# Kernel tuning notes

Measured on AMD Instinct MI355X. Metric: run time of the kernel, lower is better.

The kernel has to match this reference:

```python
import jax, jax.numpy as jnp
import numpy as np

D_MODEL = 1024
NHEAD = 16
HEAD_DIM = D_MODEL // NHEAD


def setup_inputs() -> dict:
    key = jax.random.key(0)
    ks = jax.random.split(key, 11)
    B, S, D = 4, 2048, D_MODEL
    scale = 1.0 / np.sqrt(D)
    inp = {
        'q': jax.random.normal(ks[0], (B, S, D), jnp.float32),
        'k': jax.random.normal(ks[1], (B, S, D), jnp.float32),
        'v': jax.random.normal(ks[2], (B, S, D), jnp.float32),
        'Wq': jax.random.normal(ks[3], (D, D), jnp.float32) * scale,
        'bq': jnp.zeros((D,), jnp.float32),
        'Wk': jax.random.normal(ks[4], (D, D), jnp.float32) * scale,
        'bk': jnp.zeros((D,), jnp.float32),
        'Wv': jax.random.normal(ks[5], (D, D), jnp.float32) * scale,
        'bv': jnp.zeros((D,), jnp.float32),
        'Wo': jax.random.normal(ks[6], (D, D), jnp.float32) * scale,
        'bo': jnp.zeros((D,), jnp.float32),
    }
    return inp


def reference(q, k, v, Wq, bq, Wk, bk, Wv, bv, Wo, bo):
    B, S, D = q.shape
    H, Hd = NHEAD, HEAD_DIM
    # projections (torch Linear: x @ W.T + b), then split heads -> [B,H,S,Hd]
    qh = (q @ Wq.T + bq).reshape(B, S, H, Hd).transpose(0, 2, 1, 3)
    kh = (k @ Wk.T + bk).reshape(B, S, H, Hd).transpose(0, 2, 1, 3)
    vh = (v @ Wv.T + bv).reshape(B, S, H, Hd).transpose(0, 2, 1, 3)
    # scaled dot-product attention (mask=None, dropout eval-mode identity)
    scores = jnp.einsum('bhqd,bhkd->bhqk', qh, kh) / jnp.sqrt(jnp.float32(Hd))
    attn = jax.nn.softmax(scores, axis=-1)
    out = jnp.einsum('bhqk,bhkd->bhqd', attn, vh)  # [B,H,S,Hd]
    out = out.transpose(0, 2, 1, 3).reshape(B, S, D)
    return out @ Wo.T + bo
```

## Files before the change

### kernel.cpp

```cpp
#include <hip/hip_runtime.h>
#include <cstdint>

using u16 = unsigned short;
using u32 = unsigned int;
typedef __bf16 bf16x8 __attribute__((ext_vector_type(8)));
typedef float f32x4 __attribute__((ext_vector_type(4)));
typedef float f32x16 __attribute__((ext_vector_type(16)));
typedef u16 u16x8 __attribute__((ext_vector_type(8)));
typedef u16 u16x4 __attribute__((ext_vector_type(4)));

#define DEV static __device__ __forceinline__

DEV u16 f2bf(float f) {
  uint32_t u = __builtin_bit_cast(uint32_t, f);
  u += 0x7FFFu + ((u >> 16) & 1u);
  return (u16)(u >> 16);
}
DEV float bf2f(u16 h) {
  uint32_t u = ((uint32_t)h) << 16;
  return __builtin_bit_cast(float, u);
}
DEV u32 cvt_pk_bf16(float lo, float hi) {
  u32 r;
  asm("v_cvt_pk_bf16_f32 %0, %1, %2" : "=v"(r) : "v"(lo), "v"(hi));
  return r;
}

typedef const u32 __attribute__((address_space(1))) gcu32;
typedef u32 __attribute__((address_space(3))) lu32;
DEV void gl_lds16(const u16* g, u16* l) {
  __builtin_amdgcn_global_load_lds((gcu32*)g, (lu32*)l, 16, 0, 0);
}

#define MFMA(a, b, c) __builtin_amdgcn_mfma_f32_16x16x32_bf16((a), (b), (c), 0, 0, 0)
#define MFMA32(a, b, c) __builtin_amdgcn_mfma_f32_32x32x16_bf16((a), (b), (c), 0, 0, 0)

__global__ __launch_bounds__(256) void cvt_all(
    const float* __restrict__ q, const float* __restrict__ k,
    const float* __restrict__ v, const float* __restrict__ Wq,
    const float* __restrict__ Wk, const float* __restrict__ Wv,
    const float* __restrict__ Wo, u16* __restrict__ Xb, u16* __restrict__ Wb,
    u16* __restrict__ WoB) {
  const int bid = blockIdx.x;
  const float* src;
  u16* dst;
  size_t i;
  if (bid < 12288) {
    const int z = bid >> 12;
    src = (z == 0) ? q : (z == 1) ? k : v;
    dst = Xb + (size_t)z * 8388608;
    i = ((size_t)(bid & 4095) * 256 + threadIdx.x) * 8;
  } else {
    const int r = bid - 12288;
    const int z = r >> 9;
    src = (z == 0) ? Wq : (z == 1) ? Wk : (z == 2) ? Wv : Wo;
    dst = (z < 3) ? (Wb + (size_t)z * 1048576) : WoB;
    i = ((size_t)(r & 511) * 256 + threadIdx.x) * 8;
  }
  const float4 a = *(const float4*)(src + i);
  const float4 b = *(const float4*)(src + i + 4);
  u16x8 o;
  o[0] = f2bf(a.x); o[1] = f2bf(a.y); o[2] = f2bf(a.z); o[3] = f2bf(a.w);
  o[4] = f2bf(b.x); o[5] = f2bf(b.y); o[6] = f2bf(b.z); o[7] = f2bf(b.w);
  *(u16x8*)(dst + i) = o;
}

__global__ __launch_bounds__(512) void proj_gemm_bf(
    const u16* __restrict__ Xb, const u16* __restrict__ Wb,
    const float* __restrict__ bq, const float* __restrict__ bk,
    const float* __restrict__ bv, u16* __restrict__ Qh, u16* __restrict__ Kh,
    u16* __restrict__ Vt) {
  __shared__ u16 As[256 * 64];
  __shared__ u16 Bs[128 * 64];
  const int z = blockIdx.z;
  const int m0 = blockIdx.y * 256, n0 = blockIdx.x * 128;

  const u16* x = Xb + (size_t)z * 8388608;
  const u16* W = Wb + (size_t)z * 1048576;
  const float* bias = (z == 0) ? bq : (z == 1) ? bk : bv;
  u16* out = (z == 0) ? Qh : (z == 1) ? Kh : Vt;
  const float oscale = (z == 0) ? 0.18033688011112042f : 1.0f;

  const int tid = threadIdx.x;
  const int w = tid >> 6, lane = tid & 63;
  const int wr = w >> 1, wc = w & 1;
  const int lr = lane & 15, lk = (lane >> 4) * 8;

  const u16* xg = x + (size_t)(m0 + w * 8 + (lane >> 3)) * 1024 + (lane & 7) * 8;
  const u16* wg_ = W + (size_t)(n0 + w * 8 + (lane >> 3)) * 1024 + (lane & 7) * 8;

  f32x4 acc[4][4];
  const f32x4 fzero = {0.f, 0.f, 0.f, 0.f};
#pragma unroll
  for (int m = 0; m < 4; ++m)
#pragma unroll
    for (int n = 0; n < 4; ++n) acc[m][n] = fzero;

  for (int kt = 0; kt < 16; ++kt) {
    const int k0 = kt * 64;
    __syncthreads();
#pragma unroll
    for (int c = 0; c < 4; ++c)
      gl_lds16(xg + (size_t)c * 64 * 1024 + k0, &As[c * 4096 + w * 512]);
#pragma unroll
    for (int c = 0; c < 2; ++c)
      gl_lds16(wg_ + (size_t)c * 64 * 1024 + k0, &Bs[c * 4096 + w * 512]);
    asm volatile("s_waitcnt vmcnt(0)" ::: "memory");
    __syncthreads();
#pragma unroll
    for (int kk = 0; kk < 2; ++kk) {
      bf16x8 a[4], b[4];
#pragma unroll
      for (int m = 0; m < 4; ++m)
        a[m] = *(const bf16x8*)&As[(wr * 64 + m * 16 + lr) * 64 + kk * 32 + lk];
#pragma unroll
      for (int n = 0; n < 4; ++n)
        b[n] = *(const bf16x8*)&Bs[(wc * 64 + n * 16 + lr) * 64 + kk * 32 + lk];
#pragma unroll
      for (int m = 0; m < 4; ++m)
#pragma unroll
        for (int n = 0; n < 4; ++n) acc[m][n] = MFMA(a[m], b[n], acc[m][n]);
    }
  }

#pragma unroll
  for (int n = 0; n < 4; ++n) {
    const int col = n0 + wc * 64 + n * 16 + lr;
    const float bvv = bias[col];
    const int h = col >> 6, d = col & 63;
#pragma unroll
    for (int m = 0; m < 4; ++m) {
#pragma unroll
      for (int j = 0; j < 4; ++j) {
        const int rowg = m0 + wr * 64 + m * 16 + (lane >> 4) * 4 + j;
        const int bb = rowg >> 11, s = rowg & 2047;
        const float val = (acc[m][n][j] + bvv) * oscale;
        size_t idx;
        if (z != 2)
          idx = ((size_t)(bb * 16 + h) * 2048 + s) * 64 + d;
        else
          idx = ((size_t)(bb * 16 + h) * 64 + d) * 2048 + s;
        out[idx] = f2bf(val);
      }
    }
  }
}

__global__ __launch_bounds__(256) void proj_gemm_f32(
    const float* __restrict__ q, const float* __restrict__ k,
    const float* __restrict__ v, const float* __restrict__ Wq,
    const float* __restrict__ Wk, const float* __restrict__ Wv,
    const float* __restrict__ bq, const float* __restrict__ bk,
    const float* __restrict__ bv, u16* __restrict__ Qh, u16* __restrict__ Kh,
    u16* __restrict__ Vt) {
  __shared__ u16 As[128][40];
  __shared__ u16 Bs[128][40];
  const int z = blockIdx.z;
  const float* x = (z == 0) ? q : (z == 1) ? k : v;
  const float* W = (z == 0) ? Wq : (z == 1) ? Wk : Wv;
  const float* bias = (z == 0) ? bq : (z == 1) ? bk : bv;
  u16* out = (z == 0) ? Qh : (z == 1) ? Kh : Vt;
  const float oscale = (z == 0) ? 0.18033688011112042f : 1.0f;

  const int tid = threadIdx.x;
  const int m0 = blockIdx.y * 128, n0 = blockIdx.x * 128;
  const int w = tid >> 6, lane = tid & 63;
  const int wr = w >> 1, wc = w & 1;
  const int lr = lane & 15, lk = (lane >> 4) * 8;
  const int srow = tid >> 3, sc4 = (tid & 7) * 4;

  f32x4 acc[4][4];
  const f32x4 fzero = {0.f, 0.f, 0.f, 0.f};
#pragma unroll
  for (int m = 0; m < 4; ++m)
#pragma unroll
    for (int n = 0; n < 4; ++n) acc[m][n] = fzero;

  for (int kt = 0; kt < 32; ++kt) {
    const int k0 = kt * 32;
    __syncthreads();
#pragma unroll
    for (int c = 0; c < 4; ++c) {
      const float4 av = *(const float4*)(x + (size_t)(m0 + c * 32 + srow) * 1024 + k0 + sc4);
      const float4 bvv = *(const float4*)(W + (size_t)(n0 + c * 32 + srow) * 1024 + k0 + sc4);
      u16x4 ah, bh;
      ah[0] = f2bf(av.x); ah[1] = f2bf(av.y); ah[2] = f2bf(av.z); ah[3] = f2bf(av.w);
      bh[0] = f2bf(bvv.x); bh[1] = f2bf(bvv.y); bh[2] = f2bf(bvv.z); bh[3] = f2bf(bvv.w);
      *(u16x4*)&As[c * 32 + srow][sc4] = ah;
      *(u16x4*)&Bs[c * 32 + srow][sc4] = bh;
    }
    __syncthreads();
    bf16x8 a[4], b[4];
#pragma unroll
    for (int m = 0; m < 4; ++m)
      a[m] = *(const bf16x8*)&As[wr * 64 + m * 16 + lr][lk];
#pragma unroll
    for (int n = 0; n < 4; ++n)
      b[n] = *(const bf16x8*)&Bs[wc * 64 + n * 16 + lr][lk];
#pragma unroll
    for (int m = 0; m < 4; ++m)
#pragma unroll
      for (int n = 0; n < 4; ++n) acc[m][n] = MFMA(a[m], b[n], acc[m][n]);
  }

#pragma unroll
  for (int n = 0; n < 4; ++n) {
    const int col = n0 + wc * 64 + n * 16 + lr;
    const float bvv = bias[col];
    const int h = col >> 6, d = col & 63;
#pragma unroll
    for (int m = 0; m < 4; ++m) {
#pragma unroll
      for (int j = 0; j < 4; ++j) {
        const int rowg = m0 + wr * 64 + m * 16 + (lane >> 4) * 4 + j;
        const int bb = rowg >> 11, s = rowg & 2047;
        const float val = (acc[m][n][j] + bvv) * oscale;
        size_t idx;
        if (z != 2)
          idx = ((size_t)(bb * 16 + h) * 2048 + s) * 64 + d;
        else
          idx = ((size_t)(bb * 16 + h) * 64 + d) * 2048 + s;
        out[idx] = f2bf(val);
      }
    }
  }
}

__global__ __launch_bounds__(512, 4) void attn_fwd(
    const u16* __restrict__ Qh, const u16* __restrict__ Kh,
    const u16* __restrict__ Vt, u16* __restrict__ Att) {
  __shared__ u16 Ks[64][72];
  __shared__ u16 Vs[64][72];
  const int tid = threadIdx.x;
  const int w = tid >> 6, lane = tid & 63;
  const int lq = lane & 31, h = lane >> 5;
  const int head = blockIdx.x, q0 = blockIdx.y * 256;
  const u16* Qb = Qh + (size_t)head * 131072;
  const u16* Kb = Kh + (size_t)head * 131072;
  const u16* Vb = Vt + (size_t)head * 131072;
  const int qrow = q0 + w * 32 + lq;

  bf16x8 qf[4];
#pragma unroll
  for (int dc = 0; dc < 4; ++dc)
    qf[dc] = *(const bf16x8*)(Qb + (size_t)qrow * 64 + dc * 16 + h * 8);

  u16x8 ou;
#pragma unroll
  for (int j = 0; j < 8; ++j) ou[j] = 0x3F80;
  const bf16x8 ones = __builtin_bit_cast(bf16x8, ou);

  f32x16 o0 = {}, o1 = {}, osum = {};

  const int srow = tid >> 3, scol = (tid & 7) * 8;
  uint4 kr, vr;
  kr = *(const uint4*)(Kb + (size_t)srow * 64 + scol);
  vr = *(const uint4*)(Vb + (size_t)srow * 2048 + scol);

  for (int kt = 0; kt < 32; ++kt) {
    __syncthreads();
    *(uint4*)&Ks[srow][scol] = kr;
    *(uint4*)&Vs[srow][scol] = vr;
    __syncthreads();
    if (kt + 1 < 32) {
      const int t0n = (kt + 1) * 64;
      kr = *(const uint4*)(Kb + (size_t)(t0n + srow) * 64 + scol);
      vr = *(const uint4*)(Vb + (size_t)srow * 2048 + t0n + scol);
    }

    f32x16 s0 = {}, s1 = {};
    __builtin_amdgcn_s_setprio(1);
#pragma unroll
    for (int dc = 0; dc < 4; ++dc) {
      const bf16x8 k0 = *(const bf16x8*)&Ks[lq][dc * 16 + h * 8];
      const bf16x8 k1 = *(const bf16x8*)&Ks[32 + lq][dc * 16 + h * 8];
      s0 = MFMA32(k0, qf[dc], s0);
      s1 = MFMA32(k1, qf[dc], s1);
    }
    __builtin_amdgcn_s_setprio(0);

#pragma unroll
    for (int r = 0; r < 16; ++r) {
      s0[r] = __builtin_amdgcn_exp2f(s0[r]);
      s1[r] = __builtin_amdgcn_exp2f(s1[r]);
    }

    u32 w0[8], w1[8];
#pragma unroll
    for (int b = 0; b < 4; ++b)
#pragma unroll
      for (int e = 0; e < 2; ++e) {
        w0[b * 2 + e] = cvt_pk_bf16(s0[4 * b + 2 * e], s0[4 * b + 2 * e + 1]);
        w1[b * 2 + e] = cvt_pk_bf16(s1[4 * b + 2 * e], s1[4 * b + 2 * e + 1]);
      }

    bf16x8 pa[4];
#pragma unroll
    for (int c = 0; c < 2; ++c) {
      u32 a0 = w0[(2 * c) * 2 + 0], b0 = w0[(2 * c + 1) * 2 + 0];
      u32 a1 = w0[(2 * c) * 2 + 1], b1 = w0[(2 * c + 1) * 2 + 1];
      asm("v_permlane32_swap_b32 %0, %1" : "+v"(a0), "+v"(b0));
      asm("v_permlane32_swap_b32 %0, %1" : "+v"(a1), "+v"(b1));
      const uint4 f = {a0, a1, b0, b1};
      pa[c] = __builtin_bit_cast(bf16x8, f);
    }
#pragma unroll
    for (int c = 0; c < 2; ++c) {
      u32 a0 = w1[(2 * c) * 2 + 0], b0 = w1[(2 * c + 1) * 2 + 0];
      u32 a1 = w1[(2 * c) * 2 + 1], b1 = w1[(2 * c + 1) * 2 + 1];
      asm("v_permlane32_swap_b32 %0, %1" : "+v"(a0), "+v"(b0));
      asm("v_permlane32_swap_b32 %0, %1" : "+v"(a1), "+v"(b1));
      const uint4 f = {a0, a1, b0, b1};
      pa[2 + c] = __builtin_bit_cast(bf16x8, f);
    }

    __builtin_amdgcn_s_setprio(1);
#pragma unroll
    for (int c = 0; c < 4; ++c) {
      const bf16x8 v0f = *(const bf16x8*)&Vs[lq][c * 16 + h * 8];
      const bf16x8 v1f = *(const bf16x8*)&Vs[32 + lq][c * 16 + h * 8];
      o0 = MFMA32(pa[c], v0f, o0);
      o1 = MFMA32(pa[c], v1f, o1);
      osum = MFMA32(pa[c], ones, osum);
    }
    __builtin_amdgcn_s_setprio(0);
  }

  const int bb = head >> 4, hh = head & 15;
#pragma unroll
  for (int r = 0; r < 16; ++r) {
    const int qr = (r & 3) + 8 * (r >> 2) + 4 * h;
    const float li = 1.0f / osum[r];
    const int qg = q0 + w * 32 + qr;
    const size_t base = ((size_t)(bb * 2048 + qg)) * 1024 + hh * 64;
    Att[base + lq] = f2bf(o0[r] * li);
    Att[base + 32 + lq] = f2bf(o1[r] * li);
  }
}

__global__ __launch_bounds__(256) void out_gemm_bf(
    const u16* __restrict__ Att, const u16* __restrict__ WoB,
    const float* __restrict__ bo, float* __restrict__ out) {
  __shared__ u16 As[128 * 64];
  __shared__ u16 Bs[128 * 64];
  const int m0 = blockIdx.y * 128, n0 = blockIdx.x * 128;
  const int tid = threadIdx.x;
  const int w = tid >> 6, lane = tid & 63;
  const int wr = w >> 1, wc = w & 1;
  const int lr = lane & 15, lk = (lane >> 4) * 8;

  const u16* ag = Att + (size_t)(m0 + w * 8 + (lane >> 3)) * 1024 + (lane & 7) * 8;
  const u16* bg = WoB + (size_t)(n0 + w * 8 + (lane >> 3)) * 1024 + (lane & 7) * 8;

  f32x4 acc[4][4];
  const f32x4 fzero = {0.f, 0.f, 0.f, 0.f};
#pragma unroll
  for (int m = 0; m < 4; ++m)
#pragma unroll
    for (int n = 0; n < 4; ++n) acc[m][n] = fzero;

  for (int kt = 0; kt < 16; ++kt) {
    const int k0 = kt * 64;
    __syncthreads();
#pragma unroll
    for (int c = 0; c < 4; ++c) {
      gl_lds16(ag + (size_t)c * 32 * 1024 + k0, &As[c * 2048 + w * 512]);
      gl_lds16(bg + (size_t)c * 32 * 1024 + k0, &Bs[c * 2048 + w * 512]);
    }
    asm volatile("s_waitcnt vmcnt(0)" ::: "memory");
    __syncthreads();
#pragma unroll
    for (int kk = 0; kk < 2; ++kk) {
      bf16x8 a[4], b[4];
#pragma unroll
      for (int m = 0; m < 4; ++m)
        a[m] = *(const bf16x8*)&As[(wr * 64 + m * 16 + lr) * 64 + kk * 32 + lk];
#pragma unroll
      for (int n = 0; n < 4; ++n)
        b[n] = *(const bf16x8*)&Bs[(wc * 64 + n * 16 + lr) * 64 + kk * 32 + lk];
#pragma unroll
      for (int m = 0; m < 4; ++m)
#pragma unroll
        for (int n = 0; n < 4; ++n) acc[m][n] = MFMA(a[m], b[n], acc[m][n]);
    }
  }

#pragma unroll
  for (int n = 0; n < 4; ++n) {
    const int col = n0 + wc * 64 + n * 16 + lr;
    const float bvv = bo[col];
#pragma unroll
    for (int m = 0; m < 4; ++m)
#pragma unroll
      for (int j = 0; j < 4; ++j) {
        const int rowg = m0 + wr * 64 + m * 16 + (lane >> 4) * 4 + j;
        out[(size_t)rowg * 1024 + col] = acc[m][n][j] + bvv;
      }
  }
}

__global__ __launch_bounds__(256) void out_gemm_f32(
    const u16* __restrict__ Att, const float* __restrict__ Wo,
    const float* __restrict__ bo, float* __restrict__ out) {
  __shared__ u16 As[128][40], Bs[128][40];
  const int tid = threadIdx.x;
  const int m0 = blockIdx.y * 128, n0 = blockIdx.x * 128;
  const int w = tid >> 6, lane = tid & 63;
  const int wr = w >> 1, wc = w & 1;
  const int lr = lane & 15, lk = (lane >> 4) * 8;
  const int arow = tid >> 2, ac8 = (tid & 3) * 8;
  const int wrow = tid >> 3, wc4 = (tid & 7) * 4;

  f32x4 acc[4][4];
  const f32x4 fzero = {0.f, 0.f, 0.f, 0.f};
#pragma unroll
  for (int m = 0; m < 4; ++m)
#pragma unroll
    for (int n = 0; n < 4; ++n) acc[m][n] = fzero;

  for (int kt = 0; kt < 32; ++kt) {
    const int k0 = kt * 32;
    __syncthreads();
#pragma unroll
    for (int c = 0; c < 2; ++c) {
      *(uint4*)&As[c * 64 + arow][ac8] =
          *(const uint4*)(Att + (size_t)(m0 + c * 64 + arow) * 1024 + k0 + ac8);
    }
#pragma unroll
    for (int c = 0; c < 4; ++c) {
      const float4 wv = *(const float4*)(Wo + (size_t)(n0 + c * 32 + wrow) * 1024 + k0 + wc4);
      u16x4 hv;
      hv[0] = f2bf(wv.x); hv[1] = f2bf(wv.y); hv[2] = f2bf(wv.z); hv[3] = f2bf(wv.w);
      *(u16x4*)&Bs[c * 32 + wrow][wc4] = hv;
    }
    __syncthreads();
    bf16x8 a[4], b[4];
#pragma unroll
    for (int m = 0; m < 4; ++m)
      a[m] = *(const bf16x8*)&As[wr * 64 + m * 16 + lr][lk];
#pragma unroll
    for (int n = 0; n < 4; ++n)
      b[n] = *(const bf16x8*)&Bs[wc * 64 + n * 16 + lr][lk];
#pragma unroll
    for (int m = 0; m < 4; ++m)
#pragma unroll
      for (int n = 0; n < 4; ++n) acc[m][n] = MFMA(a[m], b[n], acc[m][n]);
  }

#pragma unroll
  for (int n = 0; n < 4; ++n) {
    const int col = n0 + wc * 64 + n * 16 + lr;
    const float bvv = bo[col];
#pragma unroll
    for (int m = 0; m < 4; ++m)
#pragma unroll
      for (int j = 0; j < 4; ++j) {
        const int rowg = m0 + wr * 64 + m * 16 + (lane >> 4) * 4 + j;
        out[(size_t)rowg * 1024 + col] = acc[m][n][j] + bvv;
      }
  }
}

extern "C" void kernel_launch(void* const* d_in, const int* in_sizes, int n_in,
                              void* d_out, int out_size, void* d_ws, size_t ws_size,
                              hipStream_t stream) {
  const float* q  = (const float*)d_in[0];
  const float* k  = (const float*)d_in[1];
  const float* v  = (const float*)d_in[2];
  const float* Wq = (const float*)d_in[3];
  const float* bq = (const float*)d_in[4];
  const float* Wk = (const float*)d_in[5];
  const float* bk = (const float*)d_in[6];
  const float* Wv = (const float*)d_in[7];
  const float* bv = (const float*)d_in[8];
  const float* Wo = (const float*)d_in[9];
  const float* bo = (const float*)d_in[10];

  u16* ws  = (u16*)d_ws;
  u16* Qh  = ws;
  u16* Kh  = ws + (size_t)8388608;
  u16* Vt  = ws + (size_t)16777216;
  u16* Att = ws + (size_t)25165824;
  u16* Xb  = ws + (size_t)25165824;
  u16* Wb  = ws + (size_t)50331648;
  u16* WoB = ws + (size_t)53477376;
  const size_t need = (size_t)55574528 * 2;

  if (ws_size >= need) {
    cvt_all<<<dim3(14336), dim3(256), 0, stream>>>(q, k, v, Wq, Wk, Wv, Wo, Xb,
                                                   Wb, WoB);
    proj_gemm_bf<<<dim3(8, 32, 3), dim3(512), 0, stream>>>(Xb, Wb, bq, bk, bv,
                                                           Qh, Kh, Vt);
    attn_fwd<<<dim3(64, 8), dim3(512), 0, stream>>>(Qh, Kh, Vt, Att);
    out_gemm_bf<<<dim3(8, 64), dim3(256), 0, stream>>>(Att, WoB, bo,
                                                       (float*)d_out);
  } else {
    proj_gemm_f32<<<dim3(8, 64, 3), dim3(256), 0, stream>>>(
        q, k, v, Wq, Wk, Wv, bq, bk, bv, Qh, Kh, Vt);
    attn_fwd<<<dim3(64, 8), dim3(512), 0, stream>>>(Qh, Kh, Vt, Att);
    out_gemm_f32<<<dim3(8, 64), dim3(256), 0, stream>>>(Att, Wo, bo,
                                                        (float*)d_out);
  }
}
```

Before: 235.6 us.

## Double-buffer projection and output GEMM LDS tiles with XOR swizzle

Both bf16 GEMM kernels now keep two LDS buffers, so the next K-tile is loaded while MFMAs run on the current one, replacing the load-wait-compute pattern. LDS columns are XOR-swizzled on store and load to avoid bank conflicts on the fragment reads. The projection GEMM shrinks to 128x128 tiles with 256 threads and twice as many blocks. This doubles LDS per block, which may lower occupancy, and each iteration still ends with a full vmcnt(0) wait and barrier.

```diff
diff --git a/kernel.cpp b/kernel.cpp
--- a/kernel.cpp
+++ b/kernel.cpp
@@ -65,15 +65,15 @@
   *(u16x8*)(dst + i) = o;
 }
 
-__global__ __launch_bounds__(512) void proj_gemm_bf(
+__global__ __launch_bounds__(256) void proj_gemm_bf(
     const u16* __restrict__ Xb, const u16* __restrict__ Wb,
     const float* __restrict__ bq, const float* __restrict__ bk,
     const float* __restrict__ bv, u16* __restrict__ Qh, u16* __restrict__ Kh,
     u16* __restrict__ Vt) {
-  __shared__ u16 As[256 * 64];
-  __shared__ u16 Bs[128 * 64];
+  __shared__ u16 As[2][128 * 64];
+  __shared__ u16 Bs[2][128 * 64];
   const int z = blockIdx.z;
-  const int m0 = blockIdx.y * 256, n0 = blockIdx.x * 128;
+  const int m0 = blockIdx.y * 128, n0 = blockIdx.x * 128;
 
   const u16* x = Xb + (size_t)z * 8388608;
   const u16* W = Wb + (size_t)z * 1048576;
@@ -85,9 +85,12 @@
   const int w = tid >> 6, lane = tid & 63;
   const int wr = w >> 1, wc = w & 1;
   const int lr = lane & 15, lk = (lane >> 4) * 8;
-
-  const u16* xg = x + (size_t)(m0 + w * 8 + (lane >> 3)) * 1024 + (lane & 7) * 8;
-  const u16* wg_ = W + (size_t)(n0 + w * 8 + (lane >> 3)) * 1024 + (lane & 7) * 8;
+  const int hq = lane >> 4;
+
+  const int srow = w * 8 + (lane >> 3);
+  const int scol = ((lane & 7) ^ ((lane >> 3) & 7)) * 8;
+  const u16* xg = x + (size_t)(m0 + srow) * 1024 + scol;
+  const u16* wg_ = W + (size_t)(n0 + srow) * 1024 + scol;
 
   f32x4 acc[4][4];
   const f32x4 fzero = {0.f, 0.f, 0.f, 0.f};
@@ -96,32 +99,44 @@
 #pragma unroll
     for (int n = 0; n < 4; ++n) acc[m][n] = fzero;
 
+#define PROJ_STAGE(buf, k0)                                                  \
+  {                                                                          \
+    _Pragma("unroll") for (int c = 0; c < 4; ++c) {                          \
+      gl_lds16(xg + (size_t)c * 32 * 1024 + (k0), &As[buf][c * 2048 + w * 512]); \
+      gl_lds16(wg_ + (size_t)c * 32 * 1024 + (k0), &Bs[buf][c * 2048 + w * 512]); \
+    }                                                                        \
+  }
+
+  PROJ_STAGE(0, 0);
+  asm volatile("s_waitcnt vmcnt(0)" ::: "memory");
+  __syncthreads();
+
+  int cur = 0;
   for (int kt = 0; kt < 16; ++kt) {
-    const int k0 = kt * 64;
-    __syncthreads();
-#pragma unroll
-    for (int c = 0; c < 4; ++c)
-      gl_lds16(xg + (size_t)c * 64 * 1024 + k0, &As[c * 4096 + w * 512]);
-#pragma unroll
-    for (int c = 0; c < 2; ++c)
-      gl_lds16(wg_ + (size_t)c * 64 * 1024 + k0, &Bs[c * 4096 + w * 512]);
-    asm volatile("s_waitcnt vmcnt(0)" ::: "memory");
-    __syncthreads();
+    if (kt < 15) PROJ_STAGE(cur ^ 1, (kt + 1) * 64);
 #pragma unroll
     for (int kk = 0; kk < 2; ++kk) {
       bf16x8 a[4], b[4];
 #pragma unroll
+      for (int m = 0; m < 4; ++m) {
+        const int row = wr * 64 + m * 16 + lr;
+        a[m] = *(const bf16x8*)&As[cur][row * 64 + (((kk * 4 + hq) ^ (lr & 7)) * 8)];
+      }
+#pragma unroll
+      for (int n = 0; n < 4; ++n) {
+        const int row = wc * 64 + n * 16 + lr;
+        b[n] = *(const bf16x8*)&Bs[cur][row * 64 + (((kk * 4 + hq) ^ (lr & 7)) * 8)];
+      }
+#pragma unroll
       for (int m = 0; m < 4; ++m)
-        a[m] = *(const bf16x8*)&As[(wr * 64 + m * 16 + lr) * 64 + kk * 32 + lk];
-#pragma unroll
-      for (int n = 0; n < 4; ++n)
-        b[n] = *(const bf16x8*)&Bs[(wc * 64 + n * 16 + lr) * 64 + kk * 32 + lk];
-#pragma unroll
-      for (int m = 0; m < 4; ++m)
 #pragma unroll
         for (int n = 0; n < 4; ++n) acc[m][n] = MFMA(a[m], b[n], acc[m][n]);
     }
-  }
+    asm volatile("s_waitcnt vmcnt(0)" ::: "memory");
+    __syncthreads();
+    cur ^= 1;
+  }
+#undef PROJ_STAGE
 
 #pragma unroll
   for (int n = 0; n < 4; ++n) {
@@ -341,16 +356,19 @@
 __global__ __launch_bounds__(256) void out_gemm_bf(
     const u16* __restrict__ Att, const u16* __restrict__ WoB,
     const float* __restrict__ bo, float* __restrict__ out) {
-  __shared__ u16 As[128 * 64];
-  __shared__ u16 Bs[128 * 64];
+  __shared__ u16 As[2][128 * 64];
+  __shared__ u16 Bs[2][128 * 64];
   const int m0 = blockIdx.y * 128, n0 = blockIdx.x * 128;
   const int tid = threadIdx.x;
   const int w = tid >> 6, lane = tid & 63;
   const int wr = w >> 1, wc = w & 1;
-  const int lr = lane & 15, lk = (lane >> 4) * 8;
-
-  const u16* ag = Att + (size_t)(m0 + w * 8 + (lane >> 3)) * 1024 + (lane & 7) * 8;
-  const u16* bg = WoB + (size_t)(n0 + w * 8 + (lane >> 3)) * 1024 + (lane & 7) * 8;
+  const int lr = lane & 15;
+  const int hq = lane >> 4;
+
+  const int srow = w * 8 + (lane >> 3);
+  const int scol = ((lane & 7) ^ ((lane >> 3) & 7)) * 8;
+  const u16* ag = Att + (size_t)(m0 + srow) * 1024 + scol;
+  const u16* bg = WoB + (size_t)(n0 + srow) * 1024 + scol;
 
   f32x4 acc[4][4];
   const f32x4 fzero = {0.f, 0.f, 0.f, 0.f};
@@ -359,31 +377,44 @@
 #pragma unroll
     for (int n = 0; n < 4; ++n) acc[m][n] = fzero;
 
+#define OUT_STAGE(buf, k0)                                                   \
+  {                                                                          \
+    _Pragma("unroll") for (int c = 0; c < 4; ++c) {                          \
+      gl_lds16(ag + (size_t)c * 32 * 1024 + (k0), &As[buf][c * 2048 + w * 512]); \
+      gl_lds16(bg + (size_t)c * 32 * 1024 + (k0), &Bs[buf][c * 2048 + w * 512]); \
+    }                                                                        \
+  }
+
+  OUT_STAGE(0, 0);
+  asm volatile("s_waitcnt vmcnt(0)" ::: "memory");
+  __syncthreads();
+
+  int cur = 0;
   for (int kt = 0; kt < 16; ++kt) {
-    const int k0 = kt * 64;
-    __syncthreads();
-#pragma unroll
-    for (int c = 0; c < 4; ++c) {
-      gl_lds16(ag + (size_t)c * 32 * 1024 + k0, &As[c * 2048 + w * 512]);
-      gl_lds16(bg + (size_t)c * 32 * 1024 + k0, &Bs[c * 2048 + w * 512]);
-    }
-    asm volatile("s_waitcnt vmcnt(0)" ::: "memory");
-    __syncthreads();
+    if (kt < 15) OUT_STAGE(cur ^ 1, (kt + 1) * 64);
 #pragma unroll
     for (int kk = 0; kk < 2; ++kk) {
       bf16x8 a[4], b[4];
 #pragma unroll
+      for (int m = 0; m < 4; ++m) {
+        const int row = wr * 64 + m * 16 + lr;
+        a[m] = *(const bf16x8*)&As[cur][row * 64 + (((kk * 4 + hq) ^ (lr & 7)) * 8)];
+      }
+#pragma unroll
+      for (int n = 0; n < 4; ++n) {
+        const int row = wc * 64 + n * 16 + lr;
+        b[n] = *(const bf16x8*)&Bs[cur][row * 64 + (((kk * 4 + hq) ^ (lr & 7)) * 8)];
+      }
+#pragma unroll
       for (int m = 0; m < 4; ++m)
-        a[m] = *(const bf16x8*)&As[(wr * 64 + m * 16 + lr) * 64 + kk * 32 + lk];
-#pragma unroll
-      for (int n = 0; n < 4; ++n)
-        b[n] = *(const bf16x8*)&Bs[(wc * 64 + n * 16 + lr) * 64 + kk * 32 + lk];
-#pragma unroll
-      for (int m = 0; m < 4; ++m)
 #pragma unroll
         for (int n = 0; n < 4; ++n) acc[m][n] = MFMA(a[m], b[n], acc[m][n]);
     }
-  }
+    asm volatile("s_waitcnt vmcnt(0)" ::: "memory");
+    __syncthreads();
+    cur ^= 1;
+  }
+#undef OUT_STAGE
 
 #pragma unroll
   for (int n = 0; n < 4; ++n) {
@@ -489,7 +520,7 @@
   if (ws_size >= need) {
     cvt_all<<<dim3(14336), dim3(256), 0, stream>>>(q, k, v, Wq, Wk, Wv, Wo, Xb,
                                                    Wb, WoB);
-    proj_gemm_bf<<<dim3(8, 32, 3), dim3(512), 0, stream>>>(Xb, Wb, bq, bk, bv,
+    proj_gemm_bf<<<dim3(8, 64, 3), dim3(256), 0, stream>>>(Xb, Wb, bq, bk, bv,
                                                            Qh, Kh, Vt);
     attn_fwd<<<dim3(64, 8), dim3(512), 0, stream>>>(Qh, Kh, Vt, Att);
     out_gemm_bf<<<dim3(8, 64), dim3(256), 0, stream>>>(Att, WoB, bo,
```

New measurement: 237.5 us. About the same (+0.8%).

## Use 256x128 tiles with 4 waves and XOR-swizzled LDS in GEMMs

Applied to the files above, without the earlier changes.

Both bf16 GEMMs (the QKV projection and the output projection) now run 4 waves per block, each computing a 128x64 sub-tile with an 8x4 accumulator array. The projection drops from 512 threads and the output GEMM grows its M tile from 128 to 256. The LDS layout gets an XOR swizzle on the 16-byte column chunks, applied on the global-to-LDS load side and matched on the fragment reads, to remove bank conflicts. Each B fragment is reused across eight A fragments, which raises arithmetic intensity per LDS read. The cost is higher register pressure, lower occupancy, and fewer blocks for the output GEMM (256), which may underfill the GPU.

```diff
diff --git a/kernel.cpp b/kernel.cpp
--- a/kernel.cpp
+++ b/kernel.cpp
@@ -65,7 +65,7 @@
   *(u16x8*)(dst + i) = o;
 }
 
-__global__ __launch_bounds__(512) void proj_gemm_bf(
+__global__ __launch_bounds__(256) void proj_gemm_bf(
     const u16* __restrict__ Xb, const u16* __restrict__ Wb,
     const float* __restrict__ bq, const float* __restrict__ bk,
     const float* __restrict__ bv, u16* __restrict__ Qh, u16* __restrict__ Kh,
@@ -84,15 +84,18 @@
   const int tid = threadIdx.x;
   const int w = tid >> 6, lane = tid & 63;
   const int wr = w >> 1, wc = w & 1;
-  const int lr = lane & 15, lk = (lane >> 4) * 8;
-
-  const u16* xg = x + (size_t)(m0 + w * 8 + (lane >> 3)) * 1024 + (lane & 7) * 8;
-  const u16* wg_ = W + (size_t)(n0 + w * 8 + (lane >> 3)) * 1024 + (lane & 7) * 8;
-
-  f32x4 acc[4][4];
+  const int lr = lane & 15;
+  const int hq = lane >> 4;
+
+  const int srow = w * 8 + (lane >> 3);
+  const int scol = ((lane & 7) ^ ((lane >> 3) & 7)) * 8;
+  const u16* xg = x + (size_t)(m0 + srow) * 1024 + scol;
+  const u16* wg_ = W + (size_t)(n0 + srow) * 1024 + scol;
+
+  f32x4 acc[8][4];
   const f32x4 fzero = {0.f, 0.f, 0.f, 0.f};
 #pragma unroll
-  for (int m = 0; m < 4; ++m)
+  for (int m = 0; m < 8; ++m)
 #pragma unroll
     for (int n = 0; n < 4; ++n) acc[m][n] = fzero;
 
@@ -100,26 +103,29 @@
     const int k0 = kt * 64;
     __syncthreads();
 #pragma unroll
+    for (int c = 0; c < 8; ++c)
+      gl_lds16(xg + (size_t)c * 32 * 1024 + k0, &As[(c * 32 + w * 8) * 64]);
+#pragma unroll
     for (int c = 0; c < 4; ++c)
-      gl_lds16(xg + (size_t)c * 64 * 1024 + k0, &As[c * 4096 + w * 512]);
-#pragma unroll
-    for (int c = 0; c < 2; ++c)
-      gl_lds16(wg_ + (size_t)c * 64 * 1024 + k0, &Bs[c * 4096 + w * 512]);
+      gl_lds16(wg_ + (size_t)c * 32 * 1024 + k0, &Bs[(c * 32 + w * 8) * 64]);
     asm volatile("s_waitcnt vmcnt(0)" ::: "memory");
     __syncthreads();
 #pragma unroll
     for (int kk = 0; kk < 2; ++kk) {
-      bf16x8 a[4], b[4];
-#pragma unroll
-      for (int m = 0; m < 4; ++m)
-        a[m] = *(const bf16x8*)&As[(wr * 64 + m * 16 + lr) * 64 + kk * 32 + lk];
-#pragma unroll
-      for (int n = 0; n < 4; ++n)
-        b[n] = *(const bf16x8*)&Bs[(wc * 64 + n * 16 + lr) * 64 + kk * 32 + lk];
-#pragma unroll
-      for (int m = 0; m < 4; ++m)
-#pragma unroll
-        for (int n = 0; n < 4; ++n) acc[m][n] = MFMA(a[m], b[n], acc[m][n]);
+      bf16x8 b[4];
+#pragma unroll
+      for (int n = 0; n < 4; ++n) {
+        const int row = wc * 64 + n * 16 + lr;
+        b[n] = *(const bf16x8*)&Bs[row * 64 + (((kk * 4 + hq) ^ (lr & 7)) * 8)];
+      }
+#pragma unroll
+      for (int m = 0; m < 8; ++m) {
+        const int row = wr * 128 + m * 16 + lr;
+        const bf16x8 a =
+            *(const bf16x8*)&As[row * 64 + (((kk * 4 + hq) ^ (lr & 7)) * 8)];
+#pragma unroll
+        for (int n = 0; n < 4; ++n) acc[m][n] = MFMA(a, b[n], acc[m][n]);
+      }
     }
   }
 
@@ -129,10 +135,10 @@
     const float bvv = bias[col];
     const int h = col >> 6, d = col & 63;
 #pragma unroll
-    for (int m = 0; m < 4; ++m) {
+    for (int m = 0; m < 8; ++m) {
 #pragma unroll
       for (int j = 0; j < 4; ++j) {
-        const int rowg = m0 + wr * 64 + m * 16 + (lane >> 4) * 4 + j;
+        const int rowg = m0 + wr * 128 + m * 16 + hq * 4 + j;
         const int bb = rowg >> 11, s = rowg & 2047;
         const float val = (acc[m][n][j] + bvv) * oscale;
         size_t idx;
@@ -341,21 +347,24 @@
 __global__ __launch_bounds__(256) void out_gemm_bf(
     const u16* __restrict__ Att, const u16* __restrict__ WoB,
     const float* __restrict__ bo, float* __restrict__ out) {
-  __shared__ u16 As[128 * 64];
+  __shared__ u16 As[256 * 64];
   __shared__ u16 Bs[128 * 64];
-  const int m0 = blockIdx.y * 128, n0 = blockIdx.x * 128;
+  const int m0 = blockIdx.y * 256, n0 = blockIdx.x * 128;
   const int tid = threadIdx.x;
   const int w = tid >> 6, lane = tid & 63;
   const int wr = w >> 1, wc = w & 1;
-  const int lr = lane & 15, lk = (lane >> 4) * 8;
-
-  const u16* ag = Att + (size_t)(m0 + w * 8 + (lane >> 3)) * 1024 + (lane & 7) * 8;
-  const u16* bg = WoB + (size_t)(n0 + w * 8 + (lane >> 3)) * 1024 + (lane & 7) * 8;
-
-  f32x4 acc[4][4];
+  const int lr = lane & 15;
+  const int hq = lane >> 4;
+
+  const int srow = w * 8 + (lane >> 3);
+  const int scol = ((lane & 7) ^ ((lane >> 3) & 7)) * 8;
+  const u16* ag = Att + (size_t)(m0 + srow) * 1024 + scol;
+  const u16* bg = WoB + (size_t)(n0 + srow) * 1024 + scol;
+
+  f32x4 acc[8][4];
   const f32x4 fzero = {0.f, 0.f, 0.f, 0.f};
 #pragma unroll
-  for (int m = 0; m < 4; ++m)
+  for (int m = 0; m < 8; ++m)
 #pragma unroll
     for (int n = 0; n < 4; ++n) acc[m][n] = fzero;
 
@@ -363,25 +372,29 @@
     const int k0 = kt * 64;
     __syncthreads();
 #pragma unroll
-    for (int c = 0; c < 4; ++c) {
-      gl_lds16(ag + (size_t)c * 32 * 1024 + k0, &As[c * 2048 + w * 512]);
-      gl_lds16(bg + (size_t)c * 32 * 1024 + k0, &Bs[c * 2048 + w * 512]);
-    }
+    for (int c = 0; c < 8; ++c)
+      gl_lds16(ag + (size_t)c * 32 * 1024 + k0, &As[(c * 32 + w * 8) * 64]);
+#pragma unroll
+    for (int c = 0; c < 4; ++c)
+      gl_lds16(bg + (size_t)c * 32 * 1024 + k0, &Bs[(c * 32 + w * 8) * 64]);
     asm volatile("s_waitcnt vmcnt(0)" ::: "memory");
     __syncthreads();
 #pragma unroll
     for (int kk = 0; kk < 2; ++kk) {
-      bf16x8 a[4], b[4];
-#pragma unroll
-      for (int m = 0; m < 4; ++m)
-        a[m] = *(const bf16x8*)&As[(wr * 64 + m * 16 + lr) * 64 + kk * 32 + lk];
-#pragma unroll
-      for (int n = 0; n < 4; ++n)
-        b[n] = *(const bf16x8*)&Bs[(wc * 64 + n * 16 + lr) * 64 + kk * 32 + lk];
-#pragma unroll
-      for (int m = 0; m < 4; ++m)
-#pragma unroll
-        for (int n = 0; n < 4; ++n) acc[m][n] = MFMA(a[m], b[n], acc[m][n]);
+      bf16x8 b[4];
+#pragma unroll
+      for (int n = 0; n < 4; ++n) {
+        const int row = wc * 64 + n * 16 + lr;
+        b[n] = *(const bf16x8*)&Bs[row * 64 + (((kk * 4 + hq) ^ (lr & 7)) * 8)];
+      }
+#pragma unroll
+      for (int m = 0; m < 8; ++m) {
+        const int row = wr * 128 + m * 16 + lr;
+        const bf16x8 a =
+            *(const bf16x8*)&As[row * 64 + (((kk * 4 + hq) ^ (lr & 7)) * 8)];
+#pragma unroll
+        for (int n = 0; n < 4; ++n) acc[m][n] = MFMA(a, b[n], acc[m][n]);
+      }
     }
   }
 
@@ -390,10 +403,10 @@
     const int col = n0 + wc * 64 + n * 16 + lr;
     const float bvv = bo[col];
 #pragma unroll
-    for (int m = 0; m < 4; ++m)
+    for (int m = 0; m < 8; ++m)
 #pragma unroll
       for (int j = 0; j < 4; ++j) {
-        const int rowg = m0 + wr * 64 + m * 16 + (lane >> 4) * 4 + j;
+        const int rowg = m0 + wr * 128 + m * 16 + hq * 4 + j;
         out[(size_t)rowg * 1024 + col] = acc[m][n][j] + bvv;
       }
   }
@@ -489,10 +502,10 @@
   if (ws_size >= need) {
     cvt_all<<<dim3(14336), dim3(256), 0, stream>>>(q, k, v, Wq, Wk, Wv, Wo, Xb,
                                                    Wb, WoB);
-    proj_gemm_bf<<<dim3(8, 32, 3), dim3(512), 0, stream>>>(Xb, Wb, bq, bk, bv,
+    proj_gemm_bf<<<dim3(8, 32, 3), dim3(256), 0, stream>>>(Xb, Wb, bq, bk, bv,
                                                            Qh, Kh, Vt);
     attn_fwd<<<dim3(64, 8), dim3(512), 0, stream>>>(Qh, Kh, Vt, Att);
-    out_gemm_bf<<<dim3(8, 64), dim3(256), 0, stream>>>(Att, WoB, bo,
+    out_gemm_bf<<<dim3(8, 32), dim3(256), 0, stream>>>(Att, WoB, bo,
                                                        (float*)d_out);
   } else {
     proj_gemm_f32<<<dim3(8, 64, 3), dim3(256), 0, stream>>>(
```

Result: slower. 262.0 us (+11.2%).

## Triple-buffer projection and output GEMMs with swizzled LDS and async prefetch

Applied to the files above, without the earlier changes.

Both bf16 GEMMs move from a load-everything-then-compute loop to a three-stage LDS ring with K-step 32. Tiles two steps ahead are prefetched with global_load_lds and partial vmcnt waits, so memory latency overlaps the MFMA work. An XOR swizzle on the LDS column chunks is meant to avoid bank conflicts on the fragment reads. The projection GEMM also shrinks from 256x128 tiles with 512 threads to 128x128 with 256 threads, which doubles the grid but lowers per-block reuse.

```diff
diff --git a/kernel.cpp b/kernel.cpp
--- a/kernel.cpp
+++ b/kernel.cpp
@@ -34,6 +34,8 @@
 
 #define MFMA(a, b, c) __builtin_amdgcn_mfma_f32_16x16x32_bf16((a), (b), (c), 0, 0, 0)
 #define MFMA32(a, b, c) __builtin_amdgcn_mfma_f32_32x32x16_bf16((a), (b), (c), 0, 0, 0)
+
+#define WAITV(n) asm volatile("s_waitcnt vmcnt(" #n ")" ::: "memory")
 
 __global__ __launch_bounds__(256) void cvt_all(
     const float* __restrict__ q, const float* __restrict__ k,
@@ -65,15 +67,15 @@
   *(u16x8*)(dst + i) = o;
 }
 
-__global__ __launch_bounds__(512) void proj_gemm_bf(
+__global__ __launch_bounds__(256) void proj_gemm_bf(
     const u16* __restrict__ Xb, const u16* __restrict__ Wb,
     const float* __restrict__ bq, const float* __restrict__ bk,
     const float* __restrict__ bv, u16* __restrict__ Qh, u16* __restrict__ Kh,
     u16* __restrict__ Vt) {
-  __shared__ u16 As[256 * 64];
-  __shared__ u16 Bs[128 * 64];
+  __shared__ u16 As[3][128 * 32];
+  __shared__ u16 Bs[3][128 * 32];
   const int z = blockIdx.z;
-  const int m0 = blockIdx.y * 256, n0 = blockIdx.x * 128;
+  const int m0 = blockIdx.y * 128, n0 = blockIdx.x * 128;
 
   const u16* x = Xb + (size_t)z * 8388608;
   const u16* W = Wb + (size_t)z * 1048576;
@@ -84,10 +86,14 @@
   const int tid = threadIdx.x;
   const int w = tid >> 6, lane = tid & 63;
   const int wr = w >> 1, wc = w & 1;
-  const int lr = lane & 15, lk = (lane >> 4) * 8;
-
-  const u16* xg = x + (size_t)(m0 + w * 8 + (lane >> 3)) * 1024 + (lane & 7) * 8;
-  const u16* wg_ = W + (size_t)(n0 + w * 8 + (lane >> 3)) * 1024 + (lane & 7) * 8;
+  const int lr = lane & 15, hq = lane >> 4;
+
+  const int srow = w * 16 + (lane >> 2);
+  const int scol = ((lane & 3) ^ ((lane >> 3) & 3)) * 8;
+  const u16* xg = x + (size_t)(m0 + srow) * 1024 + scol;
+  const u16* wg_ = W + (size_t)(n0 + srow) * 1024 + scol;
+
+  const int rchunk = ((hq ^ ((lr >> 1) & 3)) * 8);
 
   f32x4 acc[4][4];
   const f32x4 fzero = {0.f, 0.f, 0.f, 0.f};
@@ -96,32 +102,47 @@
 #pragma unroll
     for (int n = 0; n < 4; ++n) acc[m][n] = fzero;
 
-  for (int kt = 0; kt < 16; ++kt) {
-    const int k0 = kt * 64;
-    __syncthreads();
-#pragma unroll
-    for (int c = 0; c < 4; ++c)
-      gl_lds16(xg + (size_t)c * 64 * 1024 + k0, &As[c * 4096 + w * 512]);
-#pragma unroll
-    for (int c = 0; c < 2; ++c)
-      gl_lds16(wg_ + (size_t)c * 64 * 1024 + k0, &Bs[c * 4096 + w * 512]);
-    asm volatile("s_waitcnt vmcnt(0)" ::: "memory");
-    __syncthreads();
-#pragma unroll
-    for (int kk = 0; kk < 2; ++kk) {
-      bf16x8 a[4], b[4];
-#pragma unroll
-      for (int m = 0; m < 4; ++m)
-        a[m] = *(const bf16x8*)&As[(wr * 64 + m * 16 + lr) * 64 + kk * 32 + lk];
-#pragma unroll
-      for (int n = 0; n < 4; ++n)
-        b[n] = *(const bf16x8*)&Bs[(wc * 64 + n * 16 + lr) * 64 + kk * 32 + lk];
-#pragma unroll
-      for (int m = 0; m < 4; ++m)
-#pragma unroll
-        for (int n = 0; n < 4; ++n) acc[m][n] = MFMA(a[m], b[n], acc[m][n]);
-    }
-  }
+#define PSTAGE(b, t)                                                          \
+  {                                                                           \
+    _Pragma("unroll") for (int c = 0; c < 2; ++c) {                           \
+      gl_lds16(xg + (size_t)c * 64 * 1024 + (t) * 32,                         \
+               &As[b][(c * 64 + w * 16) * 32]);                               \
+      gl_lds16(wg_ + (size_t)c * 64 * 1024 + (t) * 32,                        \
+               &Bs[b][(c * 64 + w * 16) * 32]);                               \
+    }                                                                         \
+  }
+
+  PSTAGE(0, 0);
+  PSTAGE(1, 1);
+
+#pragma unroll
+  for (int t = 0; t < 32; ++t) {
+    const int cur = t % 3;
+    if (t < 30) {
+      PSTAGE((t + 2) % 3, t + 2);
+      WAITV(8);
+    } else if (t == 30) {
+      WAITV(4);
+    } else {
+      WAITV(0);
+    }
+    __builtin_amdgcn_s_barrier();
+    __builtin_amdgcn_sched_barrier(0);
+    bf16x8 a[4], b[4];
+#pragma unroll
+    for (int m = 0; m < 4; ++m)
+      a[m] = *(const bf16x8*)&As[cur][(wr * 64 + m * 16 + lr) * 32 + rchunk];
+#pragma unroll
+    for (int n = 0; n < 4; ++n)
+      b[n] = *(const bf16x8*)&Bs[cur][(wc * 64 + n * 16 + lr) * 32 + rchunk];
+#pragma unroll
+    for (int m = 0; m < 4; ++m)
+#pragma unroll
+      for (int n = 0; n < 4; ++n) acc[m][n] = MFMA(a[m], b[n], acc[m][n]);
+    __builtin_amdgcn_sched_barrier(0);
+    __builtin_amdgcn_s_barrier();
+  }
+#undef PSTAGE
 
 #pragma unroll
   for (int n = 0; n < 4; ++n) {
@@ -132,7 +153,7 @@
     for (int m = 0; m < 4; ++m) {
 #pragma unroll
       for (int j = 0; j < 4; ++j) {
-        const int rowg = m0 + wr * 64 + m * 16 + (lane >> 4) * 4 + j;
+        const int rowg = m0 + wr * 64 + m * 16 + hq * 4 + j;
         const int bb = rowg >> 11, s = rowg & 2047;
         const float val = (acc[m][n][j] + bvv) * oscale;
         size_t idx;
@@ -341,16 +362,19 @@
 __global__ __launch_bounds__(256) void out_gemm_bf(
     const u16* __restrict__ Att, const u16* __restrict__ WoB,
     const float* __restrict__ bo, float* __restrict__ out) {
-  __shared__ u16 As[128 * 64];
-  __shared__ u16 Bs[128 * 64];
+  __shared__ u16 As[3][128 * 32];
+  __shared__ u16 Bs[3][128 * 32];
   const int m0 = blockIdx.y * 128, n0 = blockIdx.x * 128;
   const int tid = threadIdx.x;
   const int w = tid >> 6, lane = tid & 63;
   const int wr = w >> 1, wc = w & 1;
-  const int lr = lane & 15, lk = (lane >> 4) * 8;
-
-  const u16* ag = Att + (size_t)(m0 + w * 8 + (lane >> 3)) * 1024 + (lane & 7) * 8;
-  const u16* bg = WoB + (size_t)(n0 + w * 8 + (lane >> 3)) * 1024 + (lane & 7) * 8;
+  const int lr = lane & 15, hq = lane >> 4;
+
+  const int srow = w * 16 + (lane >> 2);
+  const int scol = ((lane & 3) ^ ((lane >> 3) & 3)) * 8;
+  const u16* ag = Att + (size_t)(m0 + srow) * 1024 + scol;
+  const u16* bg = WoB + (size_t)(n0 + srow) * 1024 + scol;
+  const int rchunk = ((hq ^ ((lr >> 1) & 3)) * 8);
 
   f32x4 acc[4][4];
   const f32x4 fzero = {0.f, 0.f, 0.f, 0.f};
@@ -359,31 +383,47 @@
 #pragma unroll
     for (int n = 0; n < 4; ++n) acc[m][n] = fzero;
 
-  for (int kt = 0; kt < 16; ++kt) {
-    const int k0 = kt * 64;
-    __syncthreads();
-#pragma unroll
-    for (int c = 0; c < 4; ++c) {
-      gl_lds16(ag + (size_t)c * 32 * 1024 + k0, &As[c * 2048 + w * 512]);
-      gl_lds16(bg + (size_t)c * 32 * 1024 + k0, &Bs[c * 2048 + w * 512]);
-    }
-    asm volatile("s_waitcnt vmcnt(0)" ::: "memory");
-    __syncthreads();
-#pragma unroll
-    for (int kk = 0; kk < 2; ++kk) {
-      bf16x8 a[4], b[4];
-#pragma unroll
-      for (int m = 0; m < 4; ++m)
-        a[m] = *(const bf16x8*)&As[(wr * 64 + m * 16 + lr) * 64 + kk * 32 + lk];
-#pragma unroll
-      for (int n = 0; n < 4; ++n)
-        b[n] = *(const bf16x8*)&Bs[(wc * 64 + n * 16 + lr) * 64 + kk * 32 + lk];
-#pragma unroll
-      for (int m = 0; m < 4; ++m)
-#pragma unroll
-        for (int n = 0; n < 4; ++n) acc[m][n] = MFMA(a[m], b[n], acc[m][n]);
-    }
-  }
+#define OSTAGE(b, t)                                                          \
+  {                                                                           \
+    _Pragma("unroll") for (int c = 0; c < 2; ++c) {                           \
+      gl_lds16(ag + (size_t)c * 64 * 1024 + (t) * 32,                         \
+               &As[b][(c * 64 + w * 16) * 32]);                               \
+      gl_lds16(bg + (size_t)c * 64 * 1024 + (t) * 32,                         \
+               &Bs[b][(c * 64 + w * 16) * 32]);                               \
+    }                                                                         \
+  }
+
+  OSTAGE(0, 0);
+  OSTAGE(1, 1);
+
+#pragma unroll
+  for (int t = 0; t < 32; ++t) {
+    const int cur = t % 3;
+    if (t < 30) {
+      OSTAGE((t + 2) % 3, t + 2);
+      WAITV(8);
+    } else if (t == 30) {
+      WAITV(4);
+    } else {
+      WAITV(0);
+    }
+    __builtin_amdgcn_s_barrier();
+    __builtin_amdgcn_sched_barrier(0);
+    bf16x8 a[4], b[4];
+#pragma unroll
+    for (int m = 0; m < 4; ++m)
+      a[m] = *(const bf16x8*)&As[cur][(wr * 64 + m * 16 + lr) * 32 + rchunk];
+#pragma unroll
+    for (int n = 0; n < 4; ++n)
+      b[n] = *(const bf16x8*)&Bs[cur][(wc * 64 + n * 16 + lr) * 32 + rchunk];
+#pragma unroll
+    for (int m = 0; m < 4; ++m)
+#pragma unroll
+      for (int n = 0; n < 4; ++n) acc[m][n] = MFMA(a[m], b[n], acc[m][n]);
+    __builtin_amdgcn_sched_barrier(0);
+    __builtin_amdgcn_s_barrier();
+  }
+#undef OSTAGE
 
 #pragma unroll
   for (int n = 0; n < 4; ++n) {
@@ -393,7 +433,7 @@
     for (int m = 0; m < 4; ++m)
 #pragma unroll
       for (int j = 0; j < 4; ++j) {
-        const int rowg = m0 + wr * 64 + m * 16 + (lane >> 4) * 4 + j;
+        const int rowg = m0 + wr * 64 + m * 16 + hq * 4 + j;
         out[(size_t)rowg * 1024 + col] = acc[m][n][j] + bvv;
       }
   }
@@ -489,7 +529,7 @@
   if (ws_size >= need) {
     cvt_all<<<dim3(14336), dim3(256), 0, stream>>>(q, k, v, Wq, Wk, Wv, Wo, Xb,
                                                    Wb, WoB);
-    proj_gemm_bf<<<dim3(8, 32, 3), dim3(512), 0, stream>>>(Xb, Wb, bq, bk, bv,
+    proj_gemm_bf<<<dim3(8, 64, 3), dim3(256), 0, stream>>>(Xb, Wb, bq, bk, bv,
                                                            Qh, Kh, Vt);
     attn_fwd<<<dim3(64, 8), dim3(512), 0, stream>>>(Qh, Kh, Vt, Att);
     out_gemm_bf<<<dim3(8, 64), dim3(256), 0, stream>>>(Att, WoB, bo,
```

After: 218.2 us. 1.08x faster.
